# Optimization experiments

Hardware: AMD Instinct MI355X
Metric: run time of the kernel (lower is better)

## Reference

```python
import jax, jax.numpy as jnp
import numpy as np

N_NODES = 100000
N_EDGES = 1600000
IN_DIM = 128
OUT_DIM = 32
N_HEADS = 4


def setup_inputs() -> dict:
    key = jax.random.key(0)
    k1, k2, k3, k4, k5 = jax.random.split(key, 5)
    x = jax.random.normal(k1, (N_NODES, IN_DIM), dtype=jnp.float32)
    edge_index = jax.random.randint(k2, (2, N_EDGES), 0, N_NODES, dtype=jnp.int64)
    # torch nn.Linear weight layout: [out_features, in_features]
    W = jax.random.normal(k3, (OUT_DIM * N_HEADS, IN_DIM), dtype=jnp.float32) * (1.0 / np.sqrt(IN_DIM))
    a_left = jax.random.normal(k4, (N_HEADS, OUT_DIM), dtype=jnp.float32) * 0.01
    a_right = jax.random.normal(k5, (N_HEADS, OUT_DIM), dtype=jnp.float32) * 0.01
    return {"x": x, "edge_index": edge_index, "W": W, "a_left": a_left, "a_right": a_right}


def reference(x, edge_index, W, a_left, a_right):
    N = x.shape[0]
    H, D = a_left.shape
    # h: [N, H, D]
    h = (x @ W.T).reshape(N, H, D)
    src = edge_index[0]
    dst = edge_index[1]
    h_src = h[src]                                   # [E, H, D] gather
    h_dst = h[dst]                                   # [E, H, D] gather
    e = jnp.einsum('ehd,hd->eh', h_src, a_left) + jnp.einsum('ehd,hd->eh', h_dst, a_right)
    e = jax.nn.leaky_relu(e, negative_slope=0.2)
    e_exp = jnp.exp(e)                               # faithful: no max-subtraction, as in source
    denom = jax.ops.segment_sum(e_exp, dst, num_segments=N)   # [N, H]
    alpha = e_exp / (denom[dst] + 1e-8)              # [E, H]
    weighted = h_src * alpha[:, :, None]             # [E, H, D]
    out = jax.ops.segment_sum(weighted, dst, num_segments=N)  # [N, H, D]
    return out.reshape(N, H * D)                     # concat=True
```

## Files before the change

### kernel.cpp

```cpp
#include <hip/hip_runtime.h>
#include <hip/hip_bf16.h>


constexpr int IN_DIM = 128;
constexpr int HD     = 128;
constexpr int CSHIFT = 9;
constexpr int CCAP   = 9216;
constexpr int CPAD   = 16;
constexpr int WCOLS  = 144;

typedef float f32x4 __attribute__((ext_vector_type(4)));
typedef short short8 __attribute__((ext_vector_type(8)));

__device__ __forceinline__ unsigned short f2bf(float f) {
  __hip_bfloat16 b = __float2bfloat16(f);
  return *(unsigned short*)&b;
}
__device__ __forceinline__ float bfl(unsigned u) { return __uint_as_float(u << 16); }
__device__ __forceinline__ float bfh(unsigned u) { return __uint_as_float(u & 0xffff0000u); }

__global__ __launch_bounds__(1024)
void prep_k(const float* __restrict__ W, const float* __restrict__ a_left,
            const float* __restrict__ a_right,
            unsigned short* __restrict__ Whb, unsigned short* __restrict__ Wlb,
            int* __restrict__ ccnt) {
  const int t = threadIdx.x;
  for (int i = t; i < 256 * CPAD; i += 1024) ccnt[i] = 0;

  for (int i = t; i < 128 * 128; i += 1024) {
    float w = W[i];
    unsigned wu = __float_as_uint(w);
    unsigned short h = (unsigned short)(wu >> 16);
    float hf = __uint_as_float(wu & 0xffff0000u);
    Whb[i] = h;
    Wlb[i] = f2bf(w - hf);
  }
  {
    int vec = t >> 7;
    int k   = t & 127;
    int hd  = vec & 3;
    const float* av = (vec < 4) ? a_left : a_right;
    float s = 0.f;
    for (int d = 0; d < 32; ++d) s += av[hd * 32 + d] * W[(hd * 32 + d) * IN_DIM + k];
    unsigned su = __float_as_uint(s);
    unsigned short h = (unsigned short)(su >> 16);
    float hf = __uint_as_float(su & 0xffff0000u);
    Whb[(128 + vec) * 128 + k] = h;
    Wlb[(128 + vec) * 128 + k] = f2bf(s - hf);
  }
  for (int i = t; i < 8 * 128; i += 1024) {
    Whb[136 * 128 + i] = 0;
    Wlb[136 * 128 + i] = 0;
  }
}

__device__ __forceinline__
void gemm_role(char* xs, int gb_idx,
               const float* __restrict__ x,
               const unsigned short* __restrict__ Whb,
               const unsigned short* __restrict__ Wlb,
               unsigned int* __restrict__ hb,
               float* __restrict__ el, float* __restrict__ er, int N) {
  const int tid  = threadIdx.x;
  const int lane = tid & 63;
  const int wv   = tid >> 6;
  const int lcol = lane & 15;
  const int lk   = lane >> 4;
  const int n0   = gb_idx * 64;

#pragma unroll
  for (int i = 0; i < 8; ++i) {
    int f  = tid + 256 * i;
    int r  = f >> 5;
    int c4 = f & 31;
    int node = n0 + r;
    float4 v = make_float4(0.f, 0.f, 0.f, 0.f);
    if (node < N) v = *(const float4*)&x[(size_t)node * IN_DIM + c4 * 4];
    float vf[4] = {v.x, v.y, v.z, v.w};
    unsigned short hs[4], ls[4];
#pragma unroll
    for (int j = 0; j < 4; ++j) {
      unsigned xu = __float_as_uint(vf[j]);
      hs[j] = (unsigned short)(xu >> 16);
      float hf = __uint_as_float(xu & 0xffff0000u);
      ls[j] = f2bf(vf[j] - hf);
    }
    int sw = (c4 * 8) ^ ((r & 7) << 4);
    uint2 ph = make_uint2((unsigned)hs[0] | ((unsigned)hs[1] << 16),
                          (unsigned)hs[2] | ((unsigned)hs[3] << 16));
    uint2 pl = make_uint2((unsigned)ls[0] | ((unsigned)ls[1] << 16),
                          (unsigned)ls[2] | ((unsigned)ls[3] << 16));
    *(uint2*)&xs[r * 256 + sw]         = ph;
    *(uint2*)&xs[16384 + r * 256 + sw] = pl;
  }
  __syncthreads();

  f32x4 acc[4][2];
  f32x4 acc2[4];
#pragma unroll
  for (int rt = 0; rt < 4; ++rt) {
    acc[rt][0] = (f32x4){0.f, 0.f, 0.f, 0.f};
    acc[rt][1] = (f32x4){0.f, 0.f, 0.f, 0.f};
    acc2[rt]   = (f32x4){0.f, 0.f, 0.f, 0.f};
  }

#pragma unroll
  for (int ks = 0; ks < 4; ++ks) {
    const int kb = ks * 32 + lk * 8;
    short8 bh0 = *(const short8*)&Whb[(size_t)(wv * 32 + lcol) * 128 + kb];
    short8 bl0 = *(const short8*)&Wlb[(size_t)(wv * 32 + lcol) * 128 + kb];
    short8 bh1 = *(const short8*)&Whb[(size_t)(wv * 32 + 16 + lcol) * 128 + kb];
    short8 bl1 = *(const short8*)&Wlb[(size_t)(wv * 32 + 16 + lcol) * 128 + kb];
    short8 bh2 = {}, bl2 = {};
    if (wv == 0) {
      bh2 = *(const short8*)&Whb[(size_t)(128 + lcol) * 128 + kb];
      bl2 = *(const short8*)&Wlb[(size_t)(128 + lcol) * 128 + kb];
    }
#pragma unroll
    for (int rt = 0; rt < 4; ++rt) {
      int row = rt * 16 + lcol;
      int kbyte = ks * 64 + lk * 16;
      int ad  = row * 256 + (kbyte ^ ((row & 7) << 4));
      short8 ah = *(const short8*)&xs[ad];
      short8 al = *(const short8*)&xs[16384 + ad];
      acc[rt][0] = __builtin_amdgcn_mfma_f32_16x16x32_bf16(ah, bh0, acc[rt][0], 0, 0, 0);
      acc[rt][0] = __builtin_amdgcn_mfma_f32_16x16x32_bf16(ah, bl0, acc[rt][0], 0, 0, 0);
      acc[rt][0] = __builtin_amdgcn_mfma_f32_16x16x32_bf16(al, bh0, acc[rt][0], 0, 0, 0);
      acc[rt][1] = __builtin_amdgcn_mfma_f32_16x16x32_bf16(ah, bh1, acc[rt][1], 0, 0, 0);
      acc[rt][1] = __builtin_amdgcn_mfma_f32_16x16x32_bf16(ah, bl1, acc[rt][1], 0, 0, 0);
      acc[rt][1] = __builtin_amdgcn_mfma_f32_16x16x32_bf16(al, bh1, acc[rt][1], 0, 0, 0);
      if (wv == 0) {
        acc2[rt] = __builtin_amdgcn_mfma_f32_16x16x32_bf16(ah, bh2, acc2[rt], 0, 0, 0);
        acc2[rt] = __builtin_amdgcn_mfma_f32_16x16x32_bf16(ah, bl2, acc2[rt], 0, 0, 0);
        acc2[rt] = __builtin_amdgcn_mfma_f32_16x16x32_bf16(al, bh2, acc2[rt], 0, 0, 0);
      }
    }
  }

#pragma unroll
  for (int rt = 0; rt < 4; ++rt) {
#pragma unroll
    for (int ct = 0; ct < 2; ++ct) {
      float av[4] = {acc[rt][ct][0], acc[rt][ct][1], acc[rt][ct][2], acc[rt][ct][3]};
      float pt[4];
#pragma unroll
      for (int r = 0; r < 4; ++r) pt[r] = __shfl_xor(av[r], 1, 64);
      int col = wv * 32 + ct * 16 + lcol;
      int nb  = n0 + rt * 16 + lk * 4;
      if (!(lane & 1)) {
#pragma unroll
        for (int r = 0; r < 4; ++r) {
          int node = nb + r;
          if (node < N)
            hb[(size_t)node * 64 + (col >> 1)] =
                (unsigned)f2bf(av[r]) | ((unsigned)f2bf(pt[r]) << 16);
        }
      }
    }
    if (wv == 0 && lcol < 8) {
      float* dstp = (lcol < 4) ? el : er;
      int hd = lcol & 3;
      int nb = n0 + rt * 16 + lk * 4;
#pragma unroll
      for (int r = 0; r < 4; ++r) {
        int node = nb + r;
        if (node < N) dstp[node * 4 + hd] = acc2[rt][r];
      }
    }
  }
}

__device__ __forceinline__
void binA_role(char* smem, int ab_idx,
               const int* __restrict__ ei, int* __restrict__ ccnt,
               unsigned* __restrict__ c1buf, int E, int ncb) {
  unsigned*       staged = (unsigned*)smem;
  unsigned short* sbin   = (unsigned short*)(smem + 8192);
  int*            hist   = (int*)(smem + 12288);
  int*            loff   = (int*)(smem + 13312);
  int*            cur    = (int*)(smem + 14336);
  int*            gbase  = (int*)(smem + 15360);
  int*            lws    = (int*)(smem + 16384);
  const int t = threadIdx.x;
  const int base = ab_idx * 2048;

  hist[t] = 0;
  __syncthreads();

  int src[8], dst[8], bin[8];
#pragma unroll
  for (int i = 0; i < 8; ++i) {
    int e = base + t + 256 * i;
    if (e < E) {
      src[i] = __builtin_nontemporal_load(&ei[e]);
      dst[i] = __builtin_nontemporal_load(&ei[E + e]);
      bin[i] = dst[i] >> CSHIFT;
      atomicAdd(&hist[bin[i]], 1);
    } else bin[i] = -1;
  }
  __syncthreads();

  int v = hist[t], s = v;
#pragma unroll
  for (int d = 1; d < 64; d <<= 1) {
    int u = __shfl_up(s, d, 64);
    if ((t & 63) >= d) s += u;
  }
  if ((t & 63) == 63) lws[t >> 6] = s;
  __syncthreads();
  int prefix = 0;
  for (int i = 0; i < (t >> 6); ++i) prefix += lws[i];
  int excl = prefix + s - v;
  loff[t] = excl;
  cur[t]  = excl;
  gbase[t] = (t < ncb && v > 0) ? atomicAdd(&ccnt[t * CPAD], v) : 0;
  __syncthreads();

#pragma unroll
  for (int i = 0; i < 8; ++i) {
    if (bin[i] >= 0) {
      int p = atomicAdd(&cur[bin[i]], 1);
      staged[p] = (unsigned)src[i] | ((unsigned)(dst[i] & 511) << 17);
      sbin[p]   = (unsigned short)bin[i];
    }
  }
  __syncthreads();

  const int tot = loff[255] + hist[255];
  for (int j = t; j < tot; j += 256) {
    int b = sbin[j];
    int pos = gbase[b] + (j - loff[b]);
    if (pos < CCAP) c1buf[(size_t)b * CCAP + pos] = staged[j];
  }
}

__global__ __launch_bounds__(256)
void fused_k(const float* __restrict__ x,
             const unsigned short* __restrict__ Whb,
             const unsigned short* __restrict__ Wlb,
             unsigned int* __restrict__ hb, float* __restrict__ el,
             float* __restrict__ er, const int* __restrict__ ei,
             int* __restrict__ ccnt, unsigned* __restrict__ c1buf,
             int N, int E, int ncb, int nab) {
  __shared__ __align__(16) char smem[32768];
  const int k = blockIdx.x;
  const int twoA = 2 * nab;
  if (k < twoA && (k & 1)) {
    binA_role(smem, k >> 1, ei, ccnt, c1buf, E, ncb);
  } else {
    int gidx = (k < twoA) ? (k >> 1) : (k - nab);
    gemm_role(smem, gidx, x, Whb, Wlb, hb, el, er, N);
  }
}

__global__ __launch_bounds__(512)
void binB_k(const unsigned* __restrict__ c1buf, const int* __restrict__ ccnt,
            int* __restrict__ offsets, int* __restrict__ csr,
            int N, int ncb, int E) {
  __shared__ int hist[512];
  __shared__ int wsum[8];
  __shared__ int lws2[4];
  __shared__ int sgb;
  const int b = blockIdx.x, t = threadIdx.x;

  hist[t] = 0;

  int cv = 0, cs = 0;
  if (t < 256) {
    cv = (t < ncb) ? ccnt[t * CPAD] : 0;
    cs = cv;
#pragma unroll
    for (int d = 1; d < 64; d <<= 1) {
      int u = __shfl_up(cs, d, 64);
      if ((t & 63) >= d) cs += u;
    }
    if ((t & 63) == 63) lws2[t >> 6] = cs;
  }
  if (t == 0 && b == 0) offsets[N] = E;
  __syncthreads();
  if (t < 256) {
    int cpre = 0;
    for (int i = 0; i < (t >> 6); ++i) cpre += lws2[i];
    if (t == b) sgb = cpre + cs - cv;
  }
  __syncthreads();
  const int gb = sgb;

  int m = ccnt[b * CPAD];
  if (m > CCAP) m = CCAP;
  const unsigned* bp = c1buf + (size_t)b * CCAP;
  for (int i = t; i < m; i += 512) atomicAdd(&hist[bp[i] >> 17], 1);
  __syncthreads();

  int v = hist[t], s = v;
#pragma unroll
  for (int d = 1; d < 64; d <<= 1) {
    int u = __shfl_up(s, d, 64);
    if ((t & 63) >= d) s += u;
  }
  if ((t & 63) == 63) wsum[t >> 6] = s;
  __syncthreads();
  int prefix = 0;
  for (int w = 0; w < (t >> 6); ++w) prefix += wsum[w];
  int excl = prefix + s - v;
  int node = (b << CSHIFT) + t;
  if (node < N) offsets[node] = gb + excl;
  hist[t] = excl;
  __syncthreads();

  for (int i = t; i < m; i += 512) {
    unsigned u = bp[i];
    int r = atomicAdd(&hist[u >> 17], 1);
    csr[gb + r] = (int)(u & 0x1FFFFu);
  }
}

__global__ __launch_bounds__(256)
void agg_k(const char* __restrict__ hbc, const char* __restrict__ elc,
           const float* __restrict__ er, const int* __restrict__ offsets,
           const int* __restrict__ csr, float* __restrict__ out, int N) {
  const int wid  = (blockIdx.x * blockDim.x + threadIdx.x) >> 6;
  const int lane = threadIdx.x & 63;
  if (wid >= N) return;
  const int start = offsets[wid];
  const int end   = offsets[wid + 1];
  const int q    = lane >> 4;
  const int ql   = lane & 15;
  const int head = ql >> 2;
  const unsigned qoff = (unsigned)(ql << 4);
  const unsigned hoff = (unsigned)(head << 2);
  const float erv = er[wid * 4 + head];

  float a0=0.f,a1=0.f,a2=0.f,a3=0.f,a4=0.f,a5=0.f,a6=0.f,a7=0.f,den=0.f;

  for (int base = start; base < end; base += 64) {
    int lim = end - base; if (lim > 64) lim = 64;
    int ce  = base + lane;
    int creg = __builtin_nontemporal_load(&csr[(ce < end) ? ce : (end - 1)]);

    int i = 0;
    for (; i + 8 <= lim; i += 8) {
      int s0 = __shfl(creg, i + q, 64);
      int s1 = __shfl(creg, i + 4 + q, 64);
      uint4 h0 = *(const uint4*)(hbc + (((unsigned)s0 << 8) + qoff));
      uint4 h1 = *(const uint4*)(hbc + (((unsigned)s1 << 8) + qoff));
      float e0 = *(const float*)(elc + (((unsigned)s0 << 4) + hoff));
      float e1 = *(const float*)(elc + (((unsigned)s1 << 4) + hoff));
      float t0 = e0 + erv; t0 = (t0 > 0.f) ? t0 : 0.2f * t0;
      float t1 = e1 + erv; t1 = (t1 > 0.f) ? t1 : 0.2f * t1;
      float w0 = __expf(t0), w1 = __expf(t1);
      a0 += w0 * bfl(h0.x) + w1 * bfl(h1.x);
      a1 += w0 * bfh(h0.x) + w1 * bfh(h1.x);
      a2 += w0 * bfl(h0.y) + w1 * bfl(h1.y);
      a3 += w0 * bfh(h0.y) + w1 * bfh(h1.y);
      a4 += w0 * bfl(h0.z) + w1 * bfl(h1.z);
      a5 += w0 * bfh(h0.z) + w1 * bfh(h1.z);
      a6 += w0 * bfl(h0.w) + w1 * bfl(h1.w);
      a7 += w0 * bfh(h0.w) + w1 * bfh(h1.w);
      den += w0 + w1;
    }
    if (i < lim) {
      int i0 = i + q, i1 = i + 4 + q;
      int s0 = __shfl(creg, (i0 < lim) ? i0 : 0, 64);
      int s1 = __shfl(creg, (i1 < lim) ? i1 : 0, 64);
      uint4 h0 = *(const uint4*)(hbc + (((unsigned)s0 << 8) + qoff));
      uint4 h1 = *(const uint4*)(hbc + (((unsigned)s1 << 8) + qoff));
      float e0 = *(const float*)(elc + (((unsigned)s0 << 4) + hoff));
      float e1 = *(const float*)(elc + (((unsigned)s1 << 4) + hoff));
      float t0 = e0 + erv; t0 = (t0 > 0.f) ? t0 : 0.2f * t0;
      float t1 = e1 + erv; t1 = (t1 > 0.f) ? t1 : 0.2f * t1;
      float w0 = __expf(t0), w1 = __expf(t1);
      if (i0 >= lim) w0 = 0.f;
      if (i1 >= lim) w1 = 0.f;
      a0 += w0 * bfl(h0.x) + w1 * bfl(h1.x);
      a1 += w0 * bfh(h0.x) + w1 * bfh(h1.x);
      a2 += w0 * bfl(h0.y) + w1 * bfl(h1.y);
      a3 += w0 * bfh(h0.y) + w1 * bfh(h1.y);
      a4 += w0 * bfl(h0.z) + w1 * bfl(h1.z);
      a5 += w0 * bfh(h0.z) + w1 * bfh(h1.z);
      a6 += w0 * bfl(h0.w) + w1 * bfl(h1.w);
      a7 += w0 * bfh(h0.w) + w1 * bfh(h1.w);
      den += w0 + w1;
    }
  }

#pragma unroll
  for (int m = 16; m < 64; m <<= 1) {
    a0 += __shfl_xor(a0, m, 64);  a1 += __shfl_xor(a1, m, 64);
    a2 += __shfl_xor(a2, m, 64);  a3 += __shfl_xor(a3, m, 64);
    a4 += __shfl_xor(a4, m, 64);  a5 += __shfl_xor(a5, m, 64);
    a6 += __shfl_xor(a6, m, 64);  a7 += __shfl_xor(a7, m, 64);
    den += __shfl_xor(den, m, 64);
  }
  if (q == 0) {
    float inv = 1.f / (den + 1e-8f);
    f32x4 o0 = {a0 * inv, a1 * inv, a2 * inv, a3 * inv};
    f32x4 o1 = {a4 * inv, a5 * inv, a6 * inv, a7 * inv};
    __builtin_nontemporal_store(o0, (f32x4*)&out[(size_t)wid * HD + 8 * ql]);
    __builtin_nontemporal_store(o1, (f32x4*)&out[(size_t)wid * HD + 8 * ql + 4]);
  }
}

extern "C" void kernel_launch(void* const* d_in, const int* in_sizes, int n_in,
                              void* d_out, int out_size, void* d_ws, size_t ws_size,
                              hipStream_t stream) {
  const float* x       = (const float*)d_in[0];
  const int*   ei      = (const int*)d_in[1];
  const float* W       = (const float*)d_in[2];
  const float* a_left  = (const float*)d_in[3];
  const float* a_right = (const float*)d_in[4];
  float* out = (float*)d_out;

  const int N = in_sizes[0] / IN_DIM;
  const int E = in_sizes[1] / 2;
  const int NCB = (N + (1 << CSHIFT) - 1) >> CSHIFT;
  const int GB  = (N + 63) / 64;
  const int AB  = (E + 2047) / 2048;

  char* p = (char*)d_ws;
  unsigned int* hb = (unsigned int*)p; p += (size_t)N * 64 * sizeof(unsigned int);
  float* el      = (float*)p; p += (size_t)N * 4 * sizeof(float);
  float* er      = (float*)p; p += (size_t)N * 4 * sizeof(float);
  int*   offsets = (int*)p;   p += (size_t)(N + 4) * sizeof(int);
  int*   ccnt    = (int*)p;   p += (size_t)256 * CPAD * sizeof(int);
  unsigned short* Whb = (unsigned short*)p; p += (size_t)WCOLS * 128 * sizeof(unsigned short);
  unsigned short* Wlb = (unsigned short*)p; p += (size_t)WCOLS * 128 * sizeof(unsigned short);
  int*   csr     = (int*)p;   p += (size_t)E * sizeof(int);
  unsigned* c1buf = (unsigned*)p; p += (size_t)NCB * CCAP * sizeof(unsigned);

  prep_k<<<1, 1024, 0, stream>>>(W, a_left, a_right, Whb, Wlb, ccnt);
  fused_k<<<GB + AB, 256, 0, stream>>>(x, Whb, Wlb, hb, el, er,
                                       ei, ccnt, c1buf, N, E, NCB, AB);
  binB_k<<<NCB, 512, 0, stream>>>(c1buf, ccnt, offsets, csr, N, NCB, E);
  agg_k<<<(N + 3) / 4, 256, 0, stream>>>((const char*)hb, (const char*)el, er,
                                         offsets, csr, out, N);
}
```

Baseline: 232.5 us.

## Count per-node degrees with global atomics in binning pass; unroll aggregation to sixteen

The first binning pass now also increments a global per-node degree counter for every edge. The second pass can then build node offsets straight from those counts, which removes its shared-memory histogram pass over the coarse buckets. The counters are cleared with a memset instead of inside the prep kernel. The aggregation loop is also widened to gather four edges per quarter-wave per iteration, giving more loads in flight. The trade-off is 1.6M extra global atomics on scattered addresses plus an extra memset launch.

```diff
diff --git a/kernel.cpp b/kernel.cpp
--- a/kernel.cpp
+++ b/kernel.cpp
@@ -22,10 +22,8 @@
 __global__ __launch_bounds__(1024)
 void prep_k(const float* __restrict__ W, const float* __restrict__ a_left,
             const float* __restrict__ a_right,
-            unsigned short* __restrict__ Whb, unsigned short* __restrict__ Wlb,
-            int* __restrict__ ccnt) {
+            unsigned short* __restrict__ Whb, unsigned short* __restrict__ Wlb) {
   const int t = threadIdx.x;
-  for (int i = t; i < 256 * CPAD; i += 1024) ccnt[i] = 0;
 
   for (int i = t; i < 128 * 128; i += 1024) {
     float w = W[i];
@@ -172,8 +170,9 @@
 
 __device__ __forceinline__
 void binA_role(char* smem, int ab_idx,
-               const int* __restrict__ ei, int* __restrict__ ccnt,
-               unsigned* __restrict__ c1buf, int E, int ncb) {
+               const int* __restrict__ ei, int* __restrict__ cnt,
+               int* __restrict__ ccnt, unsigned* __restrict__ c1buf,
+               int E, int ncb) {
   unsigned*       staged = (unsigned*)smem;
   unsigned short* sbin   = (unsigned short*)(smem + 8192);
   int*            hist   = (int*)(smem + 12288);
@@ -196,6 +195,7 @@
       dst[i] = __builtin_nontemporal_load(&ei[E + e]);
       bin[i] = dst[i] >> CSHIFT;
       atomicAdd(&hist[bin[i]], 1);
+      atomicAdd(&cnt[dst[i]], 1);
     } else bin[i] = -1;
   }
   __syncthreads();
@@ -240,13 +240,14 @@
              const unsigned short* __restrict__ Wlb,
              unsigned int* __restrict__ hb, float* __restrict__ el,
              float* __restrict__ er, const int* __restrict__ ei,
-             int* __restrict__ ccnt, unsigned* __restrict__ c1buf,
+             int* __restrict__ cnt, int* __restrict__ ccnt,
+             unsigned* __restrict__ c1buf,
              int N, int E, int ncb, int nab) {
   __shared__ __align__(16) char smem[32768];
   const int k = blockIdx.x;
   const int twoA = 2 * nab;
   if (k < twoA && (k & 1)) {
-    binA_role(smem, k >> 1, ei, ccnt, c1buf, E, ncb);
+    binA_role(smem, k >> 1, ei, cnt, ccnt, c1buf, E, ncb);
   } else {
     int gidx = (k < twoA) ? (k >> 1) : (k - nab);
     gemm_role(smem, gidx, x, Whb, Wlb, hb, el, er, N);
@@ -255,15 +256,13 @@
 
 __global__ __launch_bounds__(512)
 void binB_k(const unsigned* __restrict__ c1buf, const int* __restrict__ ccnt,
-            int* __restrict__ offsets, int* __restrict__ csr,
-            int N, int ncb, int E) {
-  __shared__ int hist[512];
-  __shared__ int wsum[8];
-  __shared__ int lws2[4];
+            const int* __restrict__ cnt, int* __restrict__ offsets,
+            int* __restrict__ csr, int N, int ncb, int E) {
+  __shared__ int cur[512];
+  __shared__ int wsA[8], wsB[8];
   __shared__ int sgb;
   const int b = blockIdx.x, t = threadIdx.x;
-
-  hist[t] = 0;
+  const int w = t >> 6;
 
   int cv = 0, cs = 0;
   if (t < 256) {
@@ -274,44 +273,40 @@
       int u = __shfl_up(cs, d, 64);
       if ((t & 63) >= d) cs += u;
     }
-    if ((t & 63) == 63) lws2[t >> 6] = cs;
-  }
-  if (t == 0 && b == 0) offsets[N] = E;
+    if ((t & 63) == 63) wsA[w] = cs;
+  }
+  int v = cnt[(b << CSHIFT) + t];
+  int s = v;
+#pragma unroll
+  for (int d = 1; d < 64; d <<= 1) {
+    int u = __shfl_up(s, d, 64);
+    if ((t & 63) >= d) s += u;
+  }
+  if ((t & 63) == 63) wsB[w] = s;
+  if (b == 0 && t == 0) offsets[N] = E;
   __syncthreads();
   if (t < 256) {
     int cpre = 0;
-    for (int i = 0; i < (t >> 6); ++i) cpre += lws2[i];
+    for (int i = 0; i < w; ++i) cpre += wsA[i];
     if (t == b) sgb = cpre + cs - cv;
   }
   __syncthreads();
   const int gb = sgb;
+  int pre = 0;
+  for (int i = 0; i < w; ++i) pre += wsB[i];
+  int off = gb + pre + s - v;
+  int node = (b << CSHIFT) + t;
+  if (node < N) offsets[node] = off;
+  cur[t] = off;
+  __syncthreads();
 
   int m = ccnt[b * CPAD];
   if (m > CCAP) m = CCAP;
   const unsigned* bp = c1buf + (size_t)b * CCAP;
-  for (int i = t; i < m; i += 512) atomicAdd(&hist[bp[i] >> 17], 1);
-  __syncthreads();
-
-  int v = hist[t], s = v;
-#pragma unroll
-  for (int d = 1; d < 64; d <<= 1) {
-    int u = __shfl_up(s, d, 64);
-    if ((t & 63) >= d) s += u;
-  }
-  if ((t & 63) == 63) wsum[t >> 6] = s;
-  __syncthreads();
-  int prefix = 0;
-  for (int w = 0; w < (t >> 6); ++w) prefix += wsum[w];
-  int excl = prefix + s - v;
-  int node = (b << CSHIFT) + t;
-  if (node < N) offsets[node] = gb + excl;
-  hist[t] = excl;
-  __syncthreads();
-
   for (int i = t; i < m; i += 512) {
     unsigned u = bp[i];
-    int r = atomicAdd(&hist[u >> 17], 1);
-    csr[gb + r] = (int)(u & 0x1FFFFu);
+    int r = atomicAdd(&cur[u >> 17], 1);
+    csr[r] = (int)(u & 0x1FFFFu);
   }
 }
 
@@ -339,7 +334,35 @@
     int creg = __builtin_nontemporal_load(&csr[(ce < end) ? ce : (end - 1)]);
 
     int i = 0;
-    for (; i + 8 <= lim; i += 8) {
+    for (; i + 16 <= lim; i += 16) {
+      int s0 = __shfl(creg, i + q, 64);
+      int s1 = __shfl(creg, i + 4 + q, 64);
+      int s2 = __shfl(creg, i + 8 + q, 64);
+      int s3 = __shfl(creg, i + 12 + q, 64);
+      uint4 h0 = *(const uint4*)(hbc + (((unsigned)s0 << 8) + qoff));
+      uint4 h1 = *(const uint4*)(hbc + (((unsigned)s1 << 8) + qoff));
+      uint4 h2 = *(const uint4*)(hbc + (((unsigned)s2 << 8) + qoff));
+      uint4 h3 = *(const uint4*)(hbc + (((unsigned)s3 << 8) + qoff));
+      float e0 = *(const float*)(elc + (((unsigned)s0 << 4) + hoff));
+      float e1 = *(const float*)(elc + (((unsigned)s1 << 4) + hoff));
+      float e2 = *(const float*)(elc + (((unsigned)s2 << 4) + hoff));
+      float e3 = *(const float*)(elc + (((unsigned)s3 << 4) + hoff));
+      float t0 = e0 + erv; t0 = (t0 > 0.f) ? t0 : 0.2f * t0;
+      float t1 = e1 + erv; t1 = (t1 > 0.f) ? t1 : 0.2f * t1;
+      float t2 = e2 + erv; t2 = (t2 > 0.f) ? t2 : 0.2f * t2;
+      float t3 = e3 + erv; t3 = (t3 > 0.f) ? t3 : 0.2f * t3;
+      float w0 = __expf(t0), w1 = __expf(t1), w2 = __expf(t2), w3 = __expf(t3);
+      a0 += w0 * bfl(h0.x) + w1 * bfl(h1.x) + w2 * bfl(h2.x) + w3 * bfl(h3.x);
+      a1 += w0 * bfh(h0.x) + w1 * bfh(h1.x) + w2 * bfh(h2.x) + w3 * bfh(h3.x);
+      a2 += w0 * bfl(h0.y) + w1 * bfl(h1.y) + w2 * bfl(h2.y) + w3 * bfl(h3.y);
+      a3 += w0 * bfh(h0.y) + w1 * bfh(h1.y) + w2 * bfh(h2.y) + w3 * bfh(h3.y);
+      a4 += w0 * bfl(h0.z) + w1 * bfl(h1.z) + w2 * bfl(h2.z) + w3 * bfl(h3.z);
+      a5 += w0 * bfh(h0.z) + w1 * bfh(h1.z) + w2 * bfh(h2.z) + w3 * bfh(h3.z);
+      a6 += w0 * bfl(h0.w) + w1 * bfl(h1.w) + w2 * bfl(h2.w) + w3 * bfl(h3.w);
+      a7 += w0 * bfh(h0.w) + w1 * bfh(h1.w) + w2 * bfh(h2.w) + w3 * bfh(h3.w);
+      den += w0 + w1 + w2 + w3;
+    }
+    if (i + 8 <= lim) {
       int s0 = __shfl(creg, i + q, 64);
       int s1 = __shfl(creg, i + 4 + q, 64);
       uint4 h0 = *(const uint4*)(hbc + (((unsigned)s0 << 8) + qoff));
@@ -358,6 +381,7 @@
       a6 += w0 * bfl(h0.w) + w1 * bfl(h1.w);
       a7 += w0 * bfh(h0.w) + w1 * bfh(h1.w);
       den += w0 + w1;
+      i += 8;
     }
     if (i < lim) {
       int i0 = i + q, i1 = i + 4 + q;
@@ -414,6 +438,7 @@
   const int N = in_sizes[0] / IN_DIM;
   const int E = in_sizes[1] / 2;
   const int NCB = (N + (1 << CSHIFT) - 1) >> CSHIFT;
+  const int NPAD = NCB << CSHIFT;
   const int GB  = (N + 63) / 64;
   const int AB  = (E + 2047) / 2048;
 
@@ -422,16 +447,19 @@
   float* el      = (float*)p; p += (size_t)N * 4 * sizeof(float);
   float* er      = (float*)p; p += (size_t)N * 4 * sizeof(float);
   int*   offsets = (int*)p;   p += (size_t)(N + 4) * sizeof(int);
+  int*   cnt     = (int*)p;   p += (size_t)NPAD * sizeof(int);
   int*   ccnt    = (int*)p;   p += (size_t)256 * CPAD * sizeof(int);
   unsigned short* Whb = (unsigned short*)p; p += (size_t)WCOLS * 128 * sizeof(unsigned short);
   unsigned short* Wlb = (unsigned short*)p; p += (size_t)WCOLS * 128 * sizeof(unsigned short);
   int*   csr     = (int*)p;   p += (size_t)E * sizeof(int);
   unsigned* c1buf = (unsigned*)p; p += (size_t)NCB * CCAP * sizeof(unsigned);
 
-  prep_k<<<1, 1024, 0, stream>>>(W, a_left, a_right, Whb, Wlb, ccnt);
+  hipMemsetAsync(cnt, 0, ((size_t)NPAD + 256 * CPAD) * sizeof(int), stream);
+
+  prep_k<<<1, 1024, 0, stream>>>(W, a_left, a_right, Whb, Wlb);
   fused_k<<<GB + AB, 256, 0, stream>>>(x, Whb, Wlb, hb, el, er,
-                                       ei, ccnt, c1buf, N, E, NCB, AB);
-  binB_k<<<NCB, 512, 0, stream>>>(c1buf, ccnt, offsets, csr, N, NCB, E);
+                                       ei, cnt, ccnt, c1buf, N, E, NCB, AB);
+  binB_k<<<NCB, 512, 0, stream>>>(c1buf, ccnt, cnt, offsets, csr, N, NCB, E);
   agg_k<<<(N + 3) / 4, 256, 0, stream>>>((const char*)hb, (const char*)el, er,
                                          offsets, csr, out, N);
 }
```

Measured after the change: 273.8 us. +17.8%, slower.
